# Kernel optimization log

Measured on AMD Instinct MI355X. Metric: run time of the kernel, lower is better.

Reference implementation:

```python
import jax, jax.numpy as jnp
import numpy as np

B, T, N, F_IN, F_OUT = 8, 16, 512, 128, 64
NEG_INF = -9e15


def setup_inputs() -> dict:
    key = jax.random.key(0)
    k1, k2, k3, k4, k5 = jax.random.split(key, 5)
    x = jax.random.normal(k1, (B, T, N, F_IN), dtype=jnp.float32)
    # nn.Linear weights: FC_W [out, in], FC_a [1, 2*out], no bias
    W = jax.random.normal(k2, (F_OUT, F_IN), dtype=jnp.float32) * 0.05
    a = jax.random.normal(k3, (1, 2 * F_OUT), dtype=jnp.float32) * 0.05
    adj = jax.random.randint(k4, (N, N), 0, 2, dtype=jnp.int32)
    adj_we = jax.random.uniform(k5, (N, N), dtype=jnp.float32)
    return {"x": x, "W": W, "a": a, "adj": adj, "adj_we": adj_we}


def reference(x, W, a, adj, adj_we):
    fout = W.shape[0]
    # h = FC_W(input): [B,T,N,Fout]
    h = jnp.einsum("btnf,of->btno", x, W)
    # Additive GAT score decomposition: e[i,j] = LeakyReLU(a1.h_i + a2.h_j)
    # (equivalent to FC_a(cat([h_i, h_j])) without materializing [B,T,N,N,2F])
    a1 = a[0, :fout]
    a2 = a[0, fout:]
    src = jnp.einsum("btno,o->btn", h, a1)  # contribution of node i (repeated rows)
    dst = jnp.einsum("btno,o->btn", h, a2)  # contribution of node j (tiled rows)
    e = jax.nn.leaky_relu(src[..., :, None] + dst[..., None, :], negative_slope=0.01)
    # mask where adj <= 0, scale by edge weights, softmax over neighbors (dim=3)
    att = jnp.where(adj > 0, e, NEG_INF)
    att = att * adj_we
    att = jax.nn.softmax(att, axis=-1)
    # h_prime = attention @ h : [B,T,N,N] @ [B,T,N,Fout]
    return jnp.einsum("btij,btjo->btio", att, h)
```

## Files before the change

kernel.cpp:

```cpp
#include <hip/hip_runtime.h>
#include <hip/hip_bf16.h>

#define BTOT 128
#define NN   512
#define FIN  128
#define FOUT 64

typedef __attribute__((ext_vector_type(8))) short bf16x8;
typedef __attribute__((ext_vector_type(4))) float f32x4;

static __device__ inline ushort f2bf(float f) {
    __hip_bfloat16 h = __float2bfloat16(f);
    return *(ushort*)&h;
}
static __device__ inline float bf2f(ushort u) {
    uint v = (uint)u << 16;
    return __uint_as_float(v);
}

__global__ void k_prep_w(const float* __restrict__ W, ushort* __restrict__ Whi,
                         ushort* __restrict__ Wlo) {
    int i = blockIdx.x * 256 + threadIdx.x;
    float w = W[i];
    ushort hi = f2bf(w);
    Whi[i] = hi;
    Wlo[i] = f2bf(w - bf2f(hi));
}

__global__ __launch_bounds__(256, 4)
void k_feat(const float* __restrict__ x, const ushort* __restrict__ Whi,
            const ushort* __restrict__ Wlo, const float* __restrict__ a,
            ushort* __restrict__ ht, float* __restrict__ srcv,
            float* __restrict__ dstv, const int* __restrict__ adj,
            const float* __restrict__ we, ushort* __restrict__ cds) {
    const int t   = threadIdx.x;
    const int bid = blockIdx.x;

    if (bid >= 1024) {
        int lin = ((bid - 1024) * 256 + t) * 4;
        int i = lin >> 9, j0 = lin & 511;
        int4   a4 = *(const int4*)&adj[lin];
        float4 w4 = *(const float4*)&we[lin];
        ushort o[4];
#pragma unroll
        for (int e = 0; e < 4; ++e) {
            bool  cn = ((const int*)&a4)[e] > 0;
            float w  = ((const float*)&w4)[e];
            if (cn) {
                uint ub = __float_as_uint(w * 1.44269504f);
                uint tt = ub + 0xFFFFu + ((ub >> 17) & 1u);
                o[e] = (ushort)(((tt >> 17) << 1) | 1u);
            } else {
                o[e] = (w > 0.f) ? (ushort)0 : (ushort)1;
            }
        }
        int swz = ((((i >> 4) * 2 + (j0 >> 8)) * 8 + ((j0 >> 5) & 7)) << 9)
                + (((j0 >> 3) & 3) << 7) + ((i & 15) << 3) + (j0 & 7);
        *(uint2*)&cds[swz] = *(uint2*)&o[0];
        return;
    }

    const int bt   = bid & 127;
    const int nt   = bid >> 7;
    const int wv   = t >> 6, lane = t & 63;
    const int r    = lane & 15;
    const int kc   = lane >> 4;
    const int n0   = nt * 64 + wv * 16;

    const float* xrow = x + ((long)bt * NN + n0 + r) * FIN;

    f32x4 xv8[8];
#pragma unroll
    for (int ks = 0; ks < 4; ++ks) {
        xv8[2 * ks]     = *(const f32x4*)&xrow[ks * 32 + kc * 8];
        xv8[2 * ks + 1] = *(const f32x4*)&xrow[ks * 32 + kc * 8 + 4];
    }

    bf16x8 Ahi[4], Alo[4];
#pragma unroll
    for (int ks = 0; ks < 4; ++ks)
#pragma unroll
        for (int e = 0; e < 8; ++e) {
            float xe = (e < 4) ? xv8[2 * ks][e] : xv8[2 * ks + 1][e - 4];
            uint b = __float_as_uint(xe);
            Ahi[ks][e] = (short)(b >> 16);
            float rr = xe - __uint_as_float(b & 0xFFFF0000u);
            Alo[ks][e] = (short)(__float_as_uint(rr) >> 16);
        }

    f32x4 acc[4] = {{0,0,0,0},{0,0,0,0},{0,0,0,0},{0,0,0,0}};
#pragma unroll
    for (int ks = 0; ks < 4; ++ks)
#pragma unroll
        for (int g = 0; g < 4; ++g) {
            const int wo = (g * 16 + r) * FIN + ks * 32 + kc * 8;
            bf16x8 Bhi = *(const bf16x8*)&Whi[wo];
            bf16x8 Blo = *(const bf16x8*)&Wlo[wo];
            acc[g] = __builtin_amdgcn_mfma_f32_16x16x32_bf16(Ahi[ks], Bhi, acc[g], 0, 0, 0);
            acc[g] = __builtin_amdgcn_mfma_f32_16x16x32_bf16(Alo[ks], Bhi, acc[g], 0, 0, 0);
            acc[g] = __builtin_amdgcn_mfma_f32_16x16x32_bf16(Ahi[ks], Blo, acc[g], 0, 0, 0);
        }

    float a1g[4], a2g[4];
#pragma unroll
    for (int g = 0; g < 4; ++g) {
        a1g[g] = a[g * 16 + r];
        a2g[g] = a[FOUT + g * 16 + r];
    }
    f32x4 s1v = {0,0,0,0}, s2v = {0,0,0,0};
#pragma unroll
    for (int g = 0; g < 4; ++g)
#pragma unroll
        for (int reg = 0; reg < 4; ++reg) {
            s1v[reg] += acc[g][reg] * a1g[g];
            s2v[reg] += acc[g][reg] * a2g[g];
        }
#pragma unroll
    for (int off = 8; off; off >>= 1)
#pragma unroll
        for (int reg = 0; reg < 4; ++reg) {
            s1v[reg] += __shfl_down(s1v[reg], off, 16);
            s2v[reg] += __shfl_down(s2v[reg], off, 16);
        }
    if (r == 0) {
        float4 o1 = make_float4(s1v[0], s1v[1], s1v[2], s1v[3]);
        float4 o2 = make_float4(s2v[0], s2v[1], s2v[2], s2v[3]);
        *(float4*)&srcv[bt * NN + n0 + kc * 4] = o1;
        *(float4*)&dstv[bt * NN + n0 + kc * 4] = o2;
    }

#pragma unroll
    for (int g = 0; g < 4; ++g) {
        uint2 pk;
        pk.x = (uint)f2bf(acc[g][0]) | ((uint)f2bf(acc[g][1]) << 16);
        pk.y = (uint)f2bf(acc[g][2]) | ((uint)f2bf(acc[g][3]) << 16);
        *(uint2*)&ht[(long)bt * (FOUT * NN) + (g * 16 + r) * NN + n0 + kc * 4] = pk;
    }
}

static __device__ inline bf16x8 make_afrag(uint4 c, float4 d0, float4 d1, float si) {
    float dv[8] = {d0.x, d0.y, d0.z, d0.w, d1.x, d1.y, d1.z, d1.w};
    uint  cw[4] = {c.x, c.y, c.z, c.w};
    union { uint u[4]; bf16x8 v; } A;
#pragma unroll
    for (int q = 0; q < 4; ++q) {
        uint u = cw[q];
        float c0 = __uint_as_float((u << 16) & 0xFFFE0000u);
        float c1 = __uint_as_float(u & 0xFFFE0000u);
        float s0 = si + dv[2 * q],     lr0 = fmaxf(s0, 0.01f * s0);
        float s1 = si + dv[2 * q + 1], lr1 = fmaxf(s1, 0.01f * s1);
        float p0 = __builtin_amdgcn_exp2f(c0 * lr0);
        float p1 = __builtin_amdgcn_exp2f(c1 * lr1);
        p0 = (u & 1u)       ? p0 : 0.f;
        p1 = (u & 0x10000u) ? p1 : 0.f;
        A.u[q] = __builtin_amdgcn_perm(__float_as_uint(p1), __float_as_uint(p0),
                                       0x07060302u);
    }
    return A.v;
}

__global__ __launch_bounds__(256, 4)
void k_attn(const ushort* __restrict__ ht, const float* __restrict__ srcv,
            const float* __restrict__ dstv, const ushort* __restrict__ cds,
            float* __restrict__ out) {
    __shared__ ushort hs[64 * 256];
    __shared__ float dst_s[NN];

    const int t    = threadIdx.x;
    const int bid  = blockIdx.x;
    const int bt   = bid & 127;
    const int it   = bid >> 7;
    const int i0   = it << 6;
    const int lane = t & 63;
    const int wv   = t >> 6;
    const int r16  = lane & 15;
    const int kc   = lane >> 4;
    const int koff = kc * 8;
    const int xr   = r16 & 7;

    const int ri = i0 + wv * 16 + r16;
    const float si = srcv[bt * NN + ri];
    const ushort* cdb = cds + (((it * 4 + wv) * 2) << 12) + (lane << 3);
    const ushort* htb = ht + (long)bt * (FOUT * NN);

    for (int q = t; q < NN; q += 256) dst_s[q] = dstv[bt * NN + q];

    f32x4 ac0 = {0,0,0,0}, ac1 = {0,0,0,0}, ac2 = {0,0,0,0}, ac3 = {0,0,0,0},
          acd = {0,0,0,0};
    bf16x8 ones;
#pragma unroll
    for (int j = 0; j < 8; ++j) ones[j] = (short)0x3F80;

#pragma unroll
    for (int half = 0; half < 2; ++half) {
        uint4 cdv[8];
#pragma unroll
        for (int f = 0; f < 8; ++f)
            cdv[f] = *(const uint4*)&cdb[(half * 8 + f) << 9];

        __syncthreads();
#pragma unroll
        for (int q = 0; q < 8; ++q) {
            int idx = q * 256 + t;
            int o = idx >> 5, c8 = idx & 31;
            float4 v = *(const float4*)&htb[(o << 9) + (half << 8) + (c8 << 3)];
            *(float4*)&hs[(o << 8) + ((c8 ^ (o & 7)) << 3)] = v;
        }
        __syncthreads();

        const int jg = half * 256;
#pragma unroll
        for (int jtl = 0; jtl < 4; ++jtl) {
            const int jgc = jg + jtl * 64;
            float4 d00 = *(float4*)&dst_s[jgc + koff];
            float4 d01 = *(float4*)&dst_s[jgc + koff + 4];
            float4 d10 = *(float4*)&dst_s[jgc + 32 + koff];
            float4 d11 = *(float4*)&dst_s[jgc + 32 + koff + 4];

            bf16x8 A0 = make_afrag(cdv[2 * jtl],     d00, d01, si);
            bf16x8 A1 = make_afrag(cdv[2 * jtl + 1], d10, d11, si);

#pragma unroll
            for (int s2 = 0; s2 < 2; ++s2) {
                bf16x8 A = s2 ? A1 : A0;
                const int c8v = jtl * 8 + s2 * 4 + kc;
                const int cs  = (c8v ^ xr) << 3;
                bf16x8 b0 = *(bf16x8*)&hs[(( 0 + r16) << 8) + cs];
                bf16x8 b1 = *(bf16x8*)&hs[((16 + r16) << 8) + cs];
                bf16x8 b2 = *(bf16x8*)&hs[((32 + r16) << 8) + cs];
                bf16x8 b3 = *(bf16x8*)&hs[((48 + r16) << 8) + cs];
                __builtin_amdgcn_s_setprio(1);
                ac0 = __builtin_amdgcn_mfma_f32_16x16x32_bf16(A, b0, ac0, 0, 0, 0);
                ac1 = __builtin_amdgcn_mfma_f32_16x16x32_bf16(A, b1, ac1, 0, 0, 0);
                ac2 = __builtin_amdgcn_mfma_f32_16x16x32_bf16(A, b2, ac2, 0, 0, 0);
                ac3 = __builtin_amdgcn_mfma_f32_16x16x32_bf16(A, b3, ac3, 0, 0, 0);
                acd = __builtin_amdgcn_mfma_f32_16x16x32_bf16(A, ones, acd, 0, 0, 0);
                __builtin_amdgcn_s_setprio(0);
            }
        }
    }

    float* ob = out + ((long)bt * NN + i0 + wv * 16) * FOUT;
#pragma unroll
    for (int reg = 0; reg < 4; ++reg) {
        float inv = 1.0f / acd[reg];
        const int rw = (kc * 4 + reg) * FOUT + r16;
        __builtin_nontemporal_store(ac0[reg] * inv, &ob[rw +  0]);
        __builtin_nontemporal_store(ac1[reg] * inv, &ob[rw + 16]);
        __builtin_nontemporal_store(ac2[reg] * inv, &ob[rw + 32]);
        __builtin_nontemporal_store(ac3[reg] * inv, &ob[rw + 48]);
    }
}

extern "C" void kernel_launch(void* const* d_in, const int* in_sizes, int n_in,
                              void* d_out, int out_size, void* d_ws, size_t ws_size,
                              hipStream_t stream) {
    const float* x      = (const float*)d_in[0];
    const float* W      = (const float*)d_in[1];
    const float* a      = (const float*)d_in[2];
    const int*   adj    = (const int*)d_in[3];
    const float* adj_we = (const float*)d_in[4];
    float* out = (float*)d_out;

    ushort* Whi  = (ushort*)d_ws;
    ushort* Wlo  = Whi + FOUT * FIN;
    ushort* ht   = Wlo + FOUT * FIN;
    float*  srcv = (float*)(ht + BTOT * FOUT * NN);
    float*  dstv = srcv + BTOT * NN;
    ushort* cdsw = (ushort*)(dstv + BTOT * NN);

    hipLaunchKernelGGL(k_prep_w, dim3(32), dim3(256), 0, stream, W, Whi, Wlo);
    hipLaunchKernelGGL(k_feat, dim3(1280), dim3(256), 0, stream,
                       x, Whi, Wlo, a, ht, srcv, dstv, adj, adj_we, cdsw);
    hipLaunchKernelGGL(k_attn, dim3(1024), dim3(256), 0, stream,
                       ht, srcv, dstv, cdsw, out);
}
```

Measured before the change: 46.82 us.

## Fold W bf16 split into feature kernel and widen attention blocks to 128 rows

```diff
diff --git a/kernel.cpp b/kernel.cpp
--- a/kernel.cpp
+++ b/kernel.cpp
@@ -13,23 +13,10 @@
     __hip_bfloat16 h = __float2bfloat16(f);
     return *(ushort*)&h;
 }
-static __device__ inline float bf2f(ushort u) {
-    uint v = (uint)u << 16;
-    return __uint_as_float(v);
-}
-
-__global__ void k_prep_w(const float* __restrict__ W, ushort* __restrict__ Whi,
-                         ushort* __restrict__ Wlo) {
-    int i = blockIdx.x * 256 + threadIdx.x;
-    float w = W[i];
-    ushort hi = f2bf(w);
-    Whi[i] = hi;
-    Wlo[i] = f2bf(w - bf2f(hi));
-}
 
 __global__ __launch_bounds__(256, 4)
-void k_feat(const float* __restrict__ x, const ushort* __restrict__ Whi,
-            const ushort* __restrict__ Wlo, const float* __restrict__ a,
+void k_feat(const float* __restrict__ x, const float* __restrict__ W,
+            const float* __restrict__ a,
             ushort* __restrict__ ht, float* __restrict__ srcv,
             float* __restrict__ dstv, const int* __restrict__ adj,
             const float* __restrict__ we, ushort* __restrict__ cds) {
@@ -93,9 +80,18 @@
     for (int ks = 0; ks < 4; ++ks)
 #pragma unroll
         for (int g = 0; g < 4; ++g) {
-            const int wo = (g * 16 + r) * FIN + ks * 32 + kc * 8;
-            bf16x8 Bhi = *(const bf16x8*)&Whi[wo];
-            bf16x8 Blo = *(const bf16x8*)&Wlo[wo];
+            const float* wrow = W + (g * 16 + r) * FIN + ks * 32 + kc * 8;
+            f32x4 w0 = *(const f32x4*)&wrow[0];
+            f32x4 w1 = *(const f32x4*)&wrow[4];
+            bf16x8 Bhi, Blo;
+#pragma unroll
+            for (int e = 0; e < 8; ++e) {
+                float wе = (e < 4) ? w0[e] : w1[e - 4];
+                uint b = __float_as_uint(wе);
+                Bhi[e] = (short)(b >> 16);
+                float rr = wе - __uint_as_float(b & 0xFFFF0000u);
+                Blo[e] = (short)(__float_as_uint(rr) >> 16);
+            }
             acc[g] = __builtin_amdgcn_mfma_f32_16x16x32_bf16(Ahi[ks], Bhi, acc[g], 0, 0, 0);
             acc[g] = __builtin_amdgcn_mfma_f32_16x16x32_bf16(Alo[ks], Bhi, acc[g], 0, 0, 0);
             acc[g] = __builtin_amdgcn_mfma_f32_16x16x32_bf16(Ahi[ks], Blo, acc[g], 0, 0, 0);
@@ -159,7 +155,7 @@
     return A.v;
 }
 
-__global__ __launch_bounds__(256, 4)
+__global__ __launch_bounds__(512, 2)
 void k_attn(const ushort* __restrict__ ht, const float* __restrict__ srcv,
             const float* __restrict__ dstv, const ushort* __restrict__ cds,
             float* __restrict__ out) {
@@ -170,7 +166,7 @@
     const int bid  = blockIdx.x;
     const int bt   = bid & 127;
     const int it   = bid >> 7;
-    const int i0   = it << 6;
+    const int i0   = it << 7;
     const int lane = t & 63;
     const int wv   = t >> 6;
     const int r16  = lane & 15;
@@ -180,10 +176,10 @@
 
     const int ri = i0 + wv * 16 + r16;
     const float si = srcv[bt * NN + ri];
-    const ushort* cdb = cds + (((it * 4 + wv) * 2) << 12) + (lane << 3);
+    const ushort* cdb = cds + (((it * 8 + wv) * 2) << 12) + (lane << 3);
     const ushort* htb = ht + (long)bt * (FOUT * NN);
 
-    for (int q = t; q < NN; q += 256) dst_s[q] = dstv[bt * NN + q];
+    for (int q = t; q < NN; q += 512) dst_s[q] = dstv[bt * NN + q];
 
     f32x4 ac0 = {0,0,0,0}, ac1 = {0,0,0,0}, ac2 = {0,0,0,0}, ac3 = {0,0,0,0},
           acd = {0,0,0,0};
@@ -200,8 +196,8 @@
 
         __syncthreads();
 #pragma unroll
-        for (int q = 0; q < 8; ++q) {
-            int idx = q * 256 + t;
+        for (int q = 0; q < 4; ++q) {
+            int idx = q * 512 + t;
             int o = idx >> 5, c8 = idx & 31;
             float4 v = *(const float4*)&htb[(o << 9) + (half << 8) + (c8 << 3)];
             *(float4*)&hs[(o << 8) + ((c8 ^ (o & 7)) << 3)] = v;
@@ -262,16 +258,13 @@
     const float* adj_we = (const float*)d_in[4];
     float* out = (float*)d_out;
 
-    ushort* Whi  = (ushort*)d_ws;
-    ushort* Wlo  = Whi + FOUT * FIN;
-    ushort* ht   = Wlo + FOUT * FIN;
+    ushort* ht   = (ushort*)d_ws;
     float*  srcv = (float*)(ht + BTOT * FOUT * NN);
     float*  dstv = srcv + BTOT * NN;
     ushort* cdsw = (ushort*)(dstv + BTOT * NN);
 
-    hipLaunchKernelGGL(k_prep_w, dim3(32), dim3(256), 0, stream, W, Whi, Wlo);
     hipLaunchKernelGGL(k_feat, dim3(1280), dim3(256), 0, stream,
-                       x, Whi, Wlo, a, ht, srcv, dstv, adj, adj_we, cdsw);
-    hipLaunchKernelGGL(k_attn, dim3(1024), dim3(256), 0, stream,
+                       x, W, a, ht, srcv, dstv, adj, adj_we, cdsw);
+    hipLaunchKernelGGL(k_attn, dim3(512), dim3(512), 0, stream,
                        ht, srcv, dstv, cdsw, out);
 }
```

Result: faster. 41.60 us (-11.2%).
